# Kernel tuning notes

Measured on AMD Instinct MI355X. Metric: run time of the kernel, lower is better.

The kernel has to match this reference:

```python
import jax, jax.numpy as jnp
import numpy as np

EPS = 1e-5
NUM_GROUPS = 32


def setup_inputs() -> dict:
    key = jax.random.key(0)
    B, C, H, W = 16, 512, 32, 32
    ks = jax.random.split(key, 5)
    s = 1.0 / np.sqrt(C)  # keep attention logits well-scaled
    return {
        "x": jax.random.normal(ks[0], (B, C, H, W), jnp.float32),
        "gamma": jnp.ones((C,), jnp.float32),
        "beta": jnp.zeros((C,), jnp.float32),
        "wq": jax.random.normal(ks[1], (C, C), jnp.float32) * s,
        "bq": jnp.zeros((C,), jnp.float32),
        "wk": jax.random.normal(ks[2], (C, C), jnp.float32) * s,
        "bk": jnp.zeros((C,), jnp.float32),
        "wv": jax.random.normal(ks[3], (C, C), jnp.float32) * s,
        "bv": jnp.zeros((C,), jnp.float32),
        "wp": jax.random.normal(ks[4], (C, C), jnp.float32) * s,
        "bp": jnp.zeros((C,), jnp.float32),
    }


def _group_norm(x, gamma, beta):
    B, C, H, W = x.shape
    g = NUM_GROUPS
    xg = x.reshape(B, g, C // g, H * W)
    mu = jnp.mean(xg, axis=(2, 3), keepdims=True)
    var = jnp.mean(jnp.square(xg - mu), axis=(2, 3), keepdims=True)
    h = (xg - mu) * jax.lax.rsqrt(var + EPS)
    h = h.reshape(B, C, H, W)
    return h * gamma[None, :, None, None] + beta[None, :, None, None]


def reference(x, gamma, beta, wq, bq, wk, bk, wv, bv, wp, bp):
    B, C, H, W = x.shape
    N = H * W
    h = _group_norm(x, gamma, beta).reshape(B, C, N)  # [B,C,N]
    # 1x1 convs == per-pixel matmuls over channels
    q = jnp.einsum('oc,bcn->bon', wq, h) + bq[None, :, None]
    k = jnp.einsum('oc,bcn->bon', wk, h) + bk[None, :, None]
    v = jnp.einsum('oc,bcn->bon', wv, h) + bv[None, :, None]
    scale = int(C) ** (-0.5)
    logits = jnp.einsum('bcn,bcm->bnm', q, k) * scale  # [B,N,N]
    attn = jax.nn.softmax(logits, axis=-1)
    o = jnp.einsum('bnm,bcm->bcn', attn, v)  # [B,C,N]
    out = jnp.einsum('oc,bcn->bon', wp, o) + bp[None, :, None]
    return x + out.reshape(B, C, H, W)
```

## Files before the change

kernel.cpp:

```cpp
#include <hip/hip_runtime.h>
#include <hip/hip_bf16.h>

typedef __attribute__((ext_vector_type(8))) short bf16x8;
typedef __attribute__((ext_vector_type(4))) float f32x4;
typedef __attribute__((ext_vector_type(8))) unsigned short u16x8;
typedef __attribute__((ext_vector_type(4))) unsigned short u16x4;

static __device__ __forceinline__ unsigned short f2bf(float f) {
  __hip_bfloat16 h = __float2bfloat16(f);
  union { __hip_bfloat16 h; unsigned short u; } cv; cv.h = h; return cv.u;
}
static __device__ __forceinline__ float bf2f(unsigned short u) {
  union { unsigned int u; float f; } cv; cv.u = ((unsigned int)u) << 16; return cv.f;
}

static __device__ __forceinline__ void gload16(const unsigned short* g, unsigned short* l) {
  __builtin_amdgcn_global_load_lds((const __attribute__((address_space(1))) void*)g,
                                   (__attribute__((address_space(3))) void*)l, 16, 0, 0);
}

#define BK 64

__global__ __launch_bounds__(1024, 4) void gemm_bt(
    const unsigned short* __restrict__ A, const unsigned short* __restrict__ Bm,
    long sA, long sB, int lda, int ldb, int K,
    const float* __restrict__ bias, int bias_mode, float post_scale,
    unsigned short* __restrict__ D, long sD, int ldd)
{
  __shared__ unsigned short lA[256 * BK];
  __shared__ unsigned short lB[256 * BK];
  const int gx = gridDim.x, gy = gridDim.y;
  const int nwg = gx * gy * gridDim.z;
  int orig = blockIdx.x + gx * (blockIdx.y + gy * blockIdx.z);
  int id = (orig & 7) * (nwg >> 3) + (orig >> 3);
  const int bxi = id % gx;
  int rem = id / gx;
  const int byi = rem % gy;
  const int bz = rem / gy;

  const int tid = threadIdx.x, lane = tid & 63, wid = tid >> 6;
  const int l15 = lane & 15, lhi = lane >> 4;
  const int wr = wid >> 2, wc = wid & 3;
  const long bm = (long)byi * 256, bn = (long)bxi * 256;
  const unsigned short* Ab = A + (size_t)bz * sA + (size_t)bm * lda;
  const unsigned short* Bb = Bm + (size_t)bz * sB + (size_t)bn * ldb;
  const int NT = K >> 6;

  f32x4 acc[4][4];
  #pragma unroll
  for (int i = 0; i < 4; ++i)
    #pragma unroll
    for (int j = 0; j < 4; ++j) acc[i][j] = (f32x4){0.f, 0.f, 0.f, 0.f};

  auto stage = [&](int k0) {
    #pragma unroll
    for (int j = 0; j < 2; ++j) {
      int bi = j * 1024 + tid;
      int row = bi >> 3, sl = bi & 7;
      int kb = sl ^ (row & 7);
      gload16(Ab + (size_t)row * lda + k0 + kb * 8, &lA[(j * 1024 + wid * 64) * 8]);
    }
    #pragma unroll
    for (int j = 0; j < 2; ++j) {
      int bi = j * 1024 + tid;
      int row = bi >> 3, sl = bi & 7;
      int kb = sl ^ (row & 7);
      gload16(Bb + (size_t)row * ldb + k0 + kb * 8, &lB[(j * 1024 + wid * 64) * 8]);
    }
  };

  for (int t = 0; t < NT; ++t) {
    stage(t * BK);
    __syncthreads();
    #pragma unroll
    for (int s = 0; s < 2; ++s) {
      bf16x8 af[4], bfr[4];
      #pragma unroll
      for (int mi = 0; mi < 4; ++mi) {
        int row = wr * 64 + mi * 16 + l15;
        int sl = (s * 4 + lhi) ^ (row & 7);
        af[mi] = *(const bf16x8*)&lA[row * BK + sl * 8];
      }
      #pragma unroll
      for (int ni = 0; ni < 4; ++ni) {
        int row = wc * 64 + ni * 16 + l15;
        int sl = (s * 4 + lhi) ^ (row & 7);
        bfr[ni] = *(const bf16x8*)&lB[row * BK + sl * 8];
      }
      #pragma unroll
      for (int mi = 0; mi < 4; ++mi)
        #pragma unroll
        for (int ni = 0; ni < 4; ++ni)
          acc[mi][ni] = __builtin_amdgcn_mfma_f32_16x16x32_bf16(af[mi], bfr[ni], acc[mi][ni], 0, 0, 0);
    }
    __syncthreads();
  }

  #pragma unroll
  for (int mi = 0; mi < 4; ++mi) {
    #pragma unroll
    for (int ni = 0; ni < 4; ++ni) {
      #pragma unroll
      for (int r = 0; r < 4; ++r) {
        long row = bm + wr * 64 + mi * 16 + lhi * 4 + r;
        long col = bn + wc * 64 + ni * 16 + l15;
        float v = acc[mi][ni][r];
        if (bias_mode == 1) v += bias[row];
        else if (bias_mode == 2) v += bias[col];
        v *= post_scale;
        D[(size_t)bz * sD + (size_t)row * ldd + col] = f2bf(v);
      }
    }
  }
}

__global__ __launch_bounds__(256) void groupnorm_to_ht(
    const float* __restrict__ x, const float* __restrict__ gamma,
    const float* __restrict__ beta, unsigned short* __restrict__ ht)
{
  const int b = blockIdx.x >> 5;
  const int g = blockIdx.x & 31;
  const int tid = threadIdx.x, lane = tid & 63, wid = tid >> 6;
  const float4* xg4 = (const float4*)(x + ((size_t)b * 512 + g * 16) * 1024);
  float4 v[16];
  float s = 0.f, ss = 0.f;
  #pragma unroll
  for (int j = 0; j < 16; ++j) {
    v[j] = xg4[j * 256 + tid];
    s += v[j].x + v[j].y + v[j].z + v[j].w;
    ss += v[j].x * v[j].x + v[j].y * v[j].y + v[j].z * v[j].z + v[j].w * v[j].w;
  }
  #pragma unroll
  for (int o = 32; o; o >>= 1) { s += __shfl_xor(s, o); ss += __shfl_xor(ss, o); }
  __shared__ float red[8];
  if (lane == 0) { red[wid] = s; red[4 + wid] = ss; }
  __syncthreads();
  s = red[0] + red[1] + red[2] + red[3];
  ss = red[4] + red[5] + red[6] + red[7];
  const float mu = s * (1.f / 16384.f);
  const float var = ss * (1.f / 16384.f) - mu * mu;
  const float rsig = rsqrtf(var + 1e-5f);
  __shared__ unsigned short tile[16][1024];
  #pragma unroll
  for (int j = 0; j < 16; ++j) {
    int e = (j * 256 + tid) * 4;
    int ci = e >> 10, n = e & 1023;
    float ga = gamma[g * 16 + ci] * rsig, be = beta[g * 16 + ci];
    u16x4 o = { f2bf((v[j].x - mu) * ga + be), f2bf((v[j].y - mu) * ga + be),
                f2bf((v[j].z - mu) * ga + be), f2bf((v[j].w - mu) * ga + be) };
    *(u16x4*)&tile[ci][n] = o;
  }
  __syncthreads();
  unsigned short* hb = ht + (size_t)b * 1024 * 512 + g * 16;
  for (int rep = 0; rep < 4; ++rep) {
    int n = rep * 256 + tid;
    u16x8 lo, hi;
    #pragma unroll
    for (int ci = 0; ci < 8; ++ci) lo[ci] = tile[ci][n];
    #pragma unroll
    for (int ci = 0; ci < 8; ++ci) hi[ci] = tile[8 + ci][n];
    *(u16x8*)&hb[(size_t)n * 512] = lo;
    *(u16x8*)&hb[(size_t)n * 512 + 8] = hi;
  }
}

__global__ __launch_bounds__(256) void softmax_rows(unsigned short* __restrict__ attn)
{
  int row = blockIdx.x * 4 + (threadIdx.x >> 6);
  int lane = threadIdx.x & 63;
  unsigned short* p = attn + (size_t)row * 1024;
  u16x8 c0 = *(const u16x8*)&p[lane * 8];
  u16x8 c1 = *(const u16x8*)&p[512 + lane * 8];
  float f[16];
  #pragma unroll
  for (int j = 0; j < 8; ++j) { f[j] = bf2f(c0[j]); f[8 + j] = bf2f(c1[j]); }
  float m = f[0];
  #pragma unroll
  for (int j = 1; j < 16; ++j) m = fmaxf(m, f[j]);
  #pragma unroll
  for (int o = 32; o; o >>= 1) m = fmaxf(m, __shfl_xor(m, o));
  float sum = 0.f;
  #pragma unroll
  for (int j = 0; j < 16; ++j) { f[j] = __expf(f[j] - m); sum += f[j]; }
  #pragma unroll
  for (int o = 32; o; o >>= 1) sum += __shfl_xor(sum, o);
  float inv = 1.0f / sum;
  #pragma unroll
  for (int j = 0; j < 8; ++j) { c0[j] = f2bf(f[j] * inv); c1[j] = f2bf(f[8 + j] * inv); }
  *(u16x8*)&p[lane * 8] = c0;
  *(u16x8*)&p[512 + lane * 8] = c1;
}

__global__ __launch_bounds__(256) void residual_add(
    const float* __restrict__ x, const unsigned short* __restrict__ po,
    float* __restrict__ out)
{
  int t = blockIdx.x * 256 + threadIdx.x;
  int idx = t * 8;
  int b = idx >> 19, c = (idx >> 10) & 511, n = idx & 1023;
  u16x8 g = *(const u16x8*)&po[(size_t)c * 16384 + b * 1024 + n];
  float4 x0 = *(const float4*)&x[idx];
  float4 x1 = *(const float4*)&x[idx + 4];
  float4 o0 = { x0.x + bf2f(g[0]), x0.y + bf2f(g[1]), x0.z + bf2f(g[2]), x0.w + bf2f(g[3]) };
  float4 o1 = { x1.x + bf2f(g[4]), x1.y + bf2f(g[5]), x1.z + bf2f(g[6]), x1.w + bf2f(g[7]) };
  *(float4*)&out[idx] = o0;
  *(float4*)&out[idx + 4] = o1;
}

__global__ __launch_bounds__(256) void convert_weights(
    const float* __restrict__ wq, const float* __restrict__ wk,
    const float* __restrict__ wv, const float* __restrict__ wp,
    const float* __restrict__ bq, const float* __restrict__ bk,
    unsigned short* __restrict__ out, float* __restrict__ bqk)
{
  if (blockIdx.x == 1024) {
    int i = threadIdx.x * 4;
    if (i < 512) *(float4*)&bqk[i] = *(const float4*)&bq[i];
    else         *(float4*)&bqk[i] = *(const float4*)&bk[i - 512];
    return;
  }
  int t = blockIdx.x * 256 + threadIdx.x;
  int m = t >> 16;
  int off = (t & 65535) * 4;
  const float* src = m == 0 ? wq : m == 1 ? wk : m == 2 ? wv : wp;
  float4 v = *(const float4*)&src[off];
  u16x4 o = { f2bf(v.x), f2bf(v.y), f2bf(v.z), f2bf(v.w) };
  *(u16x4*)&out[(size_t)m * 262144 + off] = o;
}

extern "C" void kernel_launch(void* const* d_in, const int* in_sizes, int n_in,
                              void* d_out, int out_size, void* d_ws, size_t ws_size,
                              hipStream_t stream)
{
  const float* x     = (const float*)d_in[0];
  const float* gamma = (const float*)d_in[1];
  const float* beta  = (const float*)d_in[2];
  const float* wq    = (const float*)d_in[3];
  const float* bq    = (const float*)d_in[4];
  const float* wk    = (const float*)d_in[5];
  const float* bk    = (const float*)d_in[6];
  const float* wv    = (const float*)d_in[7];
  const float* bv    = (const float*)d_in[8];
  const float* wp    = (const float*)d_in[9];
  const float* bp    = (const float*)d_in[10];

  unsigned short* ws   = (unsigned short*)d_ws;
  unsigned short* w_bf = ws;
  unsigned short* ht   = w_bf + 1048576;
  unsigned short* qk   = ht + 8388608;
  unsigned short* vv2  = qk + 16777216;
  unsigned short* attn = vv2 + 8388608;
  unsigned short* ot   = attn + 16777216;
  float*          bqk  = (float*)(ot + 8388608);
  unsigned short* po   = attn;

  const float scale = 0.044194173824159216f;

  convert_weights<<<dim3(1025), dim3(256), 0, stream>>>(wq, wk, wv, wp, bq, bk, w_bf, bqk);
  groupnorm_to_ht<<<dim3(512), dim3(256), 0, stream>>>(x, gamma, beta, ht);

  gemm_bt<<<dim3(4, 64, 1), dim3(1024), 0, stream>>>(
      ht, w_bf, 0L, 0L, 512, 512, 512,
      bqk, 2, 1.0f, qk, 0L, 1024);
  gemm_bt<<<dim3(64, 2, 1), dim3(1024), 0, stream>>>(
      w_bf + 2 * 262144, ht, 0L, 0L, 512, 512, 512,
      bv, 1, 1.0f, vv2, 0L, 16384);
  gemm_bt<<<dim3(4, 4, 16), dim3(1024), 0, stream>>>(
      qk, qk + 512, 1048576L, 1048576L, 1024, 1024, 512,
      (const float*)nullptr, 0, scale, attn, 1048576L, 1024);
  softmax_rows<<<dim3(4096), dim3(256), 0, stream>>>(attn);
  gemm_bt<<<dim3(2, 4, 16), dim3(1024), 0, stream>>>(
      attn, vv2, 1048576L, 1024L, 1024, 16384, 1024,
      (const float*)nullptr, 0, 1.0f, ot, 524288L, 512);
  gemm_bt<<<dim3(64, 2, 1), dim3(1024), 0, stream>>>(
      w_bf + 3 * 262144, ot, 0L, 0L, 512, 512, 512,
      bp, 1, 1.0f, po, 0L, 16384);
  residual_add<<<dim3(4096), dim3(256), 0, stream>>>(x, po, (float*)d_out);
}
```

Baseline: 195.7 us.

## Double-buffer LDS tiles in bf16 GEMM to overlap global loads with MFMA

Splits the GEMM's shared memory into two dynamically allocated buffers and prefetches the next K tile into the alternate buffer while the current tile is consumed by MFMA instructions. This drops one barrier per iteration and aims to hide global-to-LDS load latency. It doubles LDS use to 128 KB per block, which needs a raised dynamic shared memory limit and fits only one 1024-thread block per CU.

```diff
diff --git a/kernel.cpp b/kernel.cpp
--- a/kernel.cpp
+++ b/kernel.cpp
@@ -27,8 +27,7 @@
     const float* __restrict__ bias, int bias_mode, float post_scale,
     unsigned short* __restrict__ D, long sD, int ldd)
 {
-  __shared__ unsigned short lA[256 * BK];
-  __shared__ unsigned short lB[256 * BK];
+  extern __shared__ unsigned short lds[];
   const int gx = gridDim.x, gy = gridDim.y;
   const int nwg = gx * gy * gridDim.z;
   int orig = blockIdx.x + gx * (blockIdx.y + gy * blockIdx.z);
@@ -52,26 +51,32 @@
     #pragma unroll
     for (int j = 0; j < 4; ++j) acc[i][j] = (f32x4){0.f, 0.f, 0.f, 0.f};
 
-  auto stage = [&](int k0) {
+  auto stage = [&](int buf, int k0) {
+    unsigned short* la = lds + buf * 32768;
+    unsigned short* lb = la + 16384;
     #pragma unroll
     for (int j = 0; j < 2; ++j) {
       int bi = j * 1024 + tid;
       int row = bi >> 3, sl = bi & 7;
       int kb = sl ^ (row & 7);
-      gload16(Ab + (size_t)row * lda + k0 + kb * 8, &lA[(j * 1024 + wid * 64) * 8]);
+      gload16(Ab + (size_t)row * lda + k0 + kb * 8, &la[(j * 1024 + wid * 64) * 8]);
     }
     #pragma unroll
     for (int j = 0; j < 2; ++j) {
       int bi = j * 1024 + tid;
       int row = bi >> 3, sl = bi & 7;
       int kb = sl ^ (row & 7);
-      gload16(Bb + (size_t)row * ldb + k0 + kb * 8, &lB[(j * 1024 + wid * 64) * 8]);
+      gload16(Bb + (size_t)row * ldb + k0 + kb * 8, &lb[(j * 1024 + wid * 64) * 8]);
     }
   };
 
+  stage(0, 0);
+  __syncthreads();
+  int buf = 0;
   for (int t = 0; t < NT; ++t) {
-    stage(t * BK);
-    __syncthreads();
+    if (t + 1 < NT) stage(buf ^ 1, (t + 1) * BK);
+    const unsigned short* la = lds + buf * 32768;
+    const unsigned short* lb = la + 16384;
     #pragma unroll
     for (int s = 0; s < 2; ++s) {
       bf16x8 af[4], bfr[4];
@@ -79,13 +84,13 @@
       for (int mi = 0; mi < 4; ++mi) {
         int row = wr * 64 + mi * 16 + l15;
         int sl = (s * 4 + lhi) ^ (row & 7);
-        af[mi] = *(const bf16x8*)&lA[row * BK + sl * 8];
+        af[mi] = *(const bf16x8*)&la[row * BK + sl * 8];
       }
       #pragma unroll
       for (int ni = 0; ni < 4; ++ni) {
         int row = wc * 64 + ni * 16 + l15;
         int sl = (s * 4 + lhi) ^ (row & 7);
-        bfr[ni] = *(const bf16x8*)&lB[row * BK + sl * 8];
+        bfr[ni] = *(const bf16x8*)&lb[row * BK + sl * 8];
       }
       #pragma unroll
       for (int mi = 0; mi < 4; ++mi)
@@ -94,6 +99,7 @@
           acc[mi][ni] = __builtin_amdgcn_mfma_f32_16x16x32_bf16(af[mi], bfr[ni], acc[mi][ni], 0, 0, 0);
     }
     __syncthreads();
+    buf ^= 1;
   }
 
   #pragma unroll
@@ -255,24 +261,27 @@
   unsigned short* po   = attn;
 
   const float scale = 0.044194173824159216f;
+  const int SMEM = 131072;
+  hipFuncSetAttribute(reinterpret_cast<const void*>(&gemm_bt),
+                      hipFuncAttributeMaxDynamicSharedMemorySize, SMEM);
 
   convert_weights<<<dim3(1025), dim3(256), 0, stream>>>(wq, wk, wv, wp, bq, bk, w_bf, bqk);
   groupnorm_to_ht<<<dim3(512), dim3(256), 0, stream>>>(x, gamma, beta, ht);
 
-  gemm_bt<<<dim3(4, 64, 1), dim3(1024), 0, stream>>>(
+  gemm_bt<<<dim3(4, 64, 1), dim3(1024), SMEM, stream>>>(
       ht, w_bf, 0L, 0L, 512, 512, 512,
       bqk, 2, 1.0f, qk, 0L, 1024);
-  gemm_bt<<<dim3(64, 2, 1), dim3(1024), 0, stream>>>(
+  gemm_bt<<<dim3(64, 2, 1), dim3(1024), SMEM, stream>>>(
       w_bf + 2 * 262144, ht, 0L, 0L, 512, 512, 512,
       bv, 1, 1.0f, vv2, 0L, 16384);
-  gemm_bt<<<dim3(4, 4, 16), dim3(1024), 0, stream>>>(
+  gemm_bt<<<dim3(4, 4, 16), dim3(1024), SMEM, stream>>>(
       qk, qk + 512, 1048576L, 1048576L, 1024, 1024, 512,
       (const float*)nullptr, 0, scale, attn, 1048576L, 1024);
   softmax_rows<<<dim3(4096), dim3(256), 0, stream>>>(attn);
-  gemm_bt<<<dim3(2, 4, 16), dim3(1024), 0, stream>>>(
+  gemm_bt<<<dim3(2, 4, 16), dim3(1024), SMEM, stream>>>(
       attn, vv2, 1048576L, 1024L, 1024, 16384, 1024,
       (const float*)nullptr, 0, 1.0f, ot, 524288L, 512);
-  gemm_bt<<<dim3(64, 2, 1), dim3(1024), 0, stream>>>(
+  gemm_bt<<<dim3(64, 2, 1), dim3(1024), SMEM, stream>>>(
       w_bf + 3 * 262144, ot, 0L, 0L, 512, 512, 512,
       bp, 1, 1.0f, po, 0L, 16384);
   residual_add<<<dim3(4096), dim3(256), 0, stream>>>(x, po, (float*)d_out);
```

New measurement: 175.4 us. 1.12x faster.
